# Performance work log

Measured on AMD Instinct MI355X. Metric: run time of the kernel, lower is better.

The kernel has to match this reference:

```python
import jax, jax.numpy as jnp
import numpy as np

B, S, D, H, DFF, L, V = 4, 1024, 512, 8, 2048, 6, 16000
DK = D // H


def _pos_encoding(seq, d):
    pos = jnp.arange(seq, dtype=jnp.float32)[:, None]
    div = 10000.0 ** (jnp.arange(0, d, 2, dtype=jnp.float32) / d)
    pe = jnp.zeros((seq, d), jnp.float32)
    pe = pe.at[:, ::2].set(jnp.sin(pos / div))
    pe = pe.at[:, 1::2].set(jnp.cos(pos / div))
    return pe


def _ln(x, g, b, eps=1e-5):
    mu = x.mean(-1, keepdims=True)
    var = ((x - mu) ** 2).mean(-1, keepdims=True)
    return g * (x - mu) / jnp.sqrt(var + eps) + b


def _mha(xq, xkv, w, b, mask):
    # w: [4, D, D] (q, k, v, out); b: [4, D]
    q = (xq @ w[0] + b[0]).reshape(B, -1, H, DK).transpose(0, 2, 1, 3)  # [B,H,Sq,DK]
    k = (xkv @ w[1] + b[1]).reshape(B, -1, H, DK).transpose(0, 2, 1, 3)
    v = (xkv @ w[2] + b[2]).reshape(B, -1, H, DK).transpose(0, 2, 1, 3)
    scores = jnp.einsum('bhqd,bhkd->bhqk', q, k) / jnp.sqrt(jnp.float32(DK))
    if mask is not None:
        scores = jnp.where(mask, -jnp.inf, scores)
    att = jax.nn.softmax(scores, axis=-1)
    out = jnp.einsum('bhqk,bhkd->bhqd', att, v).transpose(0, 2, 1, 3).reshape(B, -1, D)
    return out @ w[3] + b[3]


def setup_inputs() -> dict:
    key = jax.random.key(0)
    ks = jax.random.split(key, 16)
    f = lambda k, shape: jax.random.normal(k, shape, dtype=jnp.float32) * 0.02
    return {
        'src': jax.random.randint(ks[0], (B, S), 0, V, dtype=jnp.int32),
        'tgt': jax.random.randint(ks[1], (B, S), 0, V, dtype=jnp.int32),
        'tgt_mask': jnp.triu(jnp.ones((S, S), dtype=bool), k=1),  # True == masked
        'src_emb': f(ks[2], (V, D)),
        'tgt_emb': f(ks[3], (V, D)),
        'enc_attn_w': f(ks[4], (L, 4, D, D)), 'enc_attn_b': jnp.zeros((L, 4, D)),
        'enc_ffn_w1': f(ks[5], (L, D, DFF)), 'enc_ffn_b1': jnp.zeros((L, DFF)),
        'enc_ffn_w2': f(ks[6], (L, DFF, D)), 'enc_ffn_b2': jnp.zeros((L, D)),
        'enc_ln_g': jnp.ones((L, 2, D)), 'enc_ln_b': jnp.zeros((L, 2, D)),
        'dec_attn_w': f(ks[7], (L, 8, D, D)), 'dec_attn_b': jnp.zeros((L, 8, D)),
        'dec_ffn_w1': f(ks[8], (L, D, DFF)), 'dec_ffn_b1': jnp.zeros((L, DFF)),
        'dec_ffn_w2': f(ks[9], (L, DFF, D)), 'dec_ffn_b2': jnp.zeros((L, D)),
        'dec_ln_g': jnp.ones((L, 3, D)), 'dec_ln_b': jnp.zeros((L, 3, D)),
        'gen_w': f(ks[10], (D, V)), 'gen_b': jnp.zeros((V,)),
    }


def reference(src, tgt, tgt_mask, src_emb, tgt_emb,
              enc_attn_w, enc_attn_b, enc_ffn_w1, enc_ffn_b1, enc_ffn_w2, enc_ffn_b2,
              enc_ln_g, enc_ln_b,
              dec_attn_w, dec_attn_b, dec_ffn_w1, dec_ffn_b1, dec_ffn_w2, dec_ffn_b2,
              dec_ln_g, dec_ln_b, gen_w, gen_b):
    pe = _pos_encoding(S, D)
    # Encoder (dropout is identity in eval)
    x = src_emb[src] + pe
    for i in range(L):
        a = _mha(x, x, enc_attn_w[i], enc_attn_b[i], None)
        x = _ln(x + a, enc_ln_g[i, 0], enc_ln_b[i, 0])
        ff = jax.nn.relu(x @ enc_ffn_w1[i] + enc_ffn_b1[i]) @ enc_ffn_w2[i] + enc_ffn_b2[i]
        x = _ln(x + ff, enc_ln_g[i, 1], enc_ln_b[i, 1])
    # Decoder
    y = tgt_emb[tgt] + pe
    for i in range(L):
        a = _mha(y, y, dec_attn_w[i, :4], dec_attn_b[i, :4], tgt_mask)
        y = _ln(y + a, dec_ln_g[i, 0], dec_ln_b[i, 0])
        a = _mha(y, x, dec_attn_w[i, 4:], dec_attn_b[i, 4:], None)
        y = _ln(y + a, dec_ln_g[i, 1], dec_ln_b[i, 1])
        ff = jax.nn.relu(y @ dec_ffn_w1[i] + dec_ffn_b1[i]) @ dec_ffn_w2[i] + dec_ffn_b2[i]
        y = _ln(y + ff, dec_ln_g[i, 2], dec_ln_b[i, 2])
    # Generator (CrossEntropyLoss variant -> raw logits)
    return y @ gen_w + gen_b
```

## Files before the change

### kernel.cpp

```cpp
#include <hip/hip_runtime.h>
#include <hip/hip_bf16.h>
#include <math.h>

typedef __hip_bfloat16 bf16;
typedef __attribute__((ext_vector_type(8))) short          s16x8;
typedef __attribute__((ext_vector_type(8))) unsigned short u16x8;
typedef __attribute__((ext_vector_type(4))) float          f32x4;

#define B_   4
#define S_   1024
#define D_   512
#define H_   8
#define DK_  64
#define DFF_ 2048
#define L_   6
#define V_   16000
#define NT_  (B_ * S_)

__global__ void detect_kernel(const void* __restrict__ g, int* __restrict__ flag)
{
    const unsigned short* u = (const unsigned short*)g;
    *flag = (u[0] == 0x3F80 && u[1] == 0x3F80) ? 1 : 0;
}

__device__ __forceinline__ float ldw(const void* p, size_t i, int isbf)
{
    if (isbf) return __bfloat162float(((const bf16*)p)[i]);
    return ((const float*)p)[i];
}

__device__ __forceinline__ unsigned short f2b(float f)
{
    unsigned int u = __float_as_uint(f);
    return (unsigned short)((u + 0x7FFFu + ((u >> 16) & 1u)) >> 16);
}
__device__ __forceinline__ float b2f(unsigned short u)
{
    return __uint_as_float((unsigned int)u << 16);
}

__global__ __launch_bounds__(256)
void embed_kernel(const int* __restrict__ tok, const void* __restrict__ emb,
                  float* __restrict__ X, const int* __restrict__ flagp)
{
    const int isbf = *flagp;
    int idx = blockIdx.x * 256 + threadIdx.x;
    int d  = idx & (D_ - 1);
    int bs = idx >> 9;
    int s  = bs & (S_ - 1);
    int t  = tok[bs];
    float e = ldw(emb, (size_t)t * D_ + d, isbf);
    float expo = (float)(d & ~1) * (1.0f / (float)D_);
    float div  = powf(10000.0f, expo);
    float arg  = (float)s / div;
    float pe   = (d & 1) ? cosf(arg) : sinf(arg);
    X[idx] = e + pe;
}

__global__ __launch_bounds__(256)
void wconv_kernel(const void* __restrict__ W, unsigned short* __restrict__ Wt,
                  int K, int N, const int* __restrict__ flagp)
{
    __shared__ unsigned short T[64 * 72];
    const int isbf = *flagp;
    const int tid = threadIdx.x;
    const int n0 = blockIdx.x * 64, k0 = blockIdx.y * 64;
    const size_t mb = (size_t)blockIdx.z * K * N;
#pragma unroll
    for (int i = 0; i < 16; ++i) {
        int idx = i * 256 + tid;
        int kk = idx >> 6, n = idx & 63;
        unsigned short v;
        if (isbf) v = ((const unsigned short*)W)[mb + (size_t)(k0 + kk) * N + n0 + n];
        else      v = f2b(((const float*)W)[mb + (size_t)(k0 + kk) * N + n0 + n]);
        T[n * 72 + kk] = v;
    }
    __syncthreads();
#pragma unroll
    for (int j = 0; j < 2; ++j) {
        int unit = j * 256 + tid;
        int n = unit >> 3, q = unit & 7;
        *(u16x8*)&Wt[mb + (size_t)(n0 + n) * K + k0 + q * 8] =
            *(const u16x8*)&T[n * 72 + q * 8];
    }
}

template<int BM, int BN, int ABF, int WT, int OB>
__global__ __launch_bounds__(256)
void gemm2_kernel(const void* __restrict__ A,
                  const void* __restrict__ W, size_t w_off,
                  const void* __restrict__ bias, size_t b_off,
                  const float* __restrict__ res,
                  void* __restrict__ C, void* __restrict__ Cout,
                  int M, int N, int K, int relu,
                  size_t sW, size_t sO, size_t sB,
                  const int* __restrict__ flagp)
{
    constexpr int ROWU = 40;
    constexpr int FM = BM / 32;
    constexpr int FN = BN / 32;
    __shared__ __align__(16) unsigned short As[BM * ROWU];
    __shared__ __align__(16) unsigned short Bs[BN * ROWU];

    const int isbf = *flagp;
    const int tid  = threadIdx.x;
    const int lane = tid & 63;
    const int wid  = tid >> 6;
    const int wr   = wid >> 1, wc = wid & 1;
    const int l15  = lane & 15, g = lane >> 4;
    const int row0 = blockIdx.y * BM;
    const int col0 = blockIdx.x * BN;
    const int z    = blockIdx.z;
    const size_t wbase = w_off + (size_t)z * sW;

    f32x4 acc[FM][FN];
#pragma unroll
    for (int i = 0; i < FM; ++i)
#pragma unroll
        for (int j = 0; j < FN; ++j)
            acc[i][j] = (f32x4){0.f, 0.f, 0.f, 0.f};

    for (int k0 = 0; k0 < K; k0 += 32) {
        if (ABF) {
#pragma unroll
            for (int u = 0; u < BM / 64; ++u) {
                int unit = tid + u * 256;
                int r = unit >> 2, q = unit & 3;
                *(u16x8*)&As[r * ROWU + q * 8] = *(const u16x8*)
                    ((const unsigned short*)A + (size_t)(row0 + r) * K + k0 + q * 8);
            }
        } else {
#pragma unroll
            for (int u = 0; u < (BM * 4) / 256; ++u) {
                int unit = tid + u * 256;
                int r = unit >> 2, q = unit & 3;
                const float* ap = (const float*)A + (size_t)(row0 + r) * K + k0 + q * 8;
                float4 f0 = *(const float4*)ap;
                float4 f1 = *(const float4*)(ap + 4);
                u16x8 v;
                v[0] = f2b(f0.x); v[1] = f2b(f0.y); v[2] = f2b(f0.z); v[3] = f2b(f0.w);
                v[4] = f2b(f1.x); v[5] = f2b(f1.y); v[6] = f2b(f1.z); v[7] = f2b(f1.w);
                *(u16x8*)&As[r * ROWU + q * 8] = v;
            }
        }
        if (WT) {
#pragma unroll
            for (int u = 0; u < BN / 64; ++u) {
                int unit = tid + u * 256;
                int n = unit >> 2, q = unit & 3;
                *(u16x8*)&Bs[n * ROWU + q * 8] = *(const u16x8*)
                    ((const unsigned short*)W + wbase + (size_t)(col0 + n) * K + k0 + q * 8);
            }
        } else {
#pragma unroll
            for (int u = 0; u < (BN * 4) / 256; ++u) {
                int unit = tid + u * 256;
                int n = unit >> 2, q = unit & 3;
                u16x8 v;
                if (isbf) {
                    const unsigned short* wp = (const unsigned short*)W;
#pragma unroll
                    for (int j = 0; j < 8; ++j)
                        v[j] = wp[wbase + (size_t)(k0 + q * 8 + j) * N + col0 + n];
                } else {
                    const float* wp = (const float*)W;
#pragma unroll
                    for (int j = 0; j < 8; ++j)
                        v[j] = f2b(wp[wbase + (size_t)(k0 + q * 8 + j) * N + col0 + n]);
                }
                *(u16x8*)&Bs[n * ROWU + q * 8] = v;
            }
        }
        __syncthreads();

        s16x8 af[FM], bfr[FN];
#pragma unroll
        for (int mi = 0; mi < FM; ++mi) {
            int r = wr * (BM / 2) + mi * 16 + l15;
            af[mi] = *(const s16x8*)&As[r * ROWU + g * 8];
        }
#pragma unroll
        for (int ni = 0; ni < FN; ++ni) {
            int c = wc * (BN / 2) + ni * 16 + l15;
            bfr[ni] = *(const s16x8*)&Bs[c * ROWU + g * 8];
        }
#pragma unroll
        for (int mi = 0; mi < FM; ++mi)
#pragma unroll
            for (int ni = 0; ni < FN; ++ni)
                acc[mi][ni] = __builtin_amdgcn_mfma_f32_16x16x32_bf16(
                    af[mi], bfr[ni], acc[mi][ni], 0, 0, 0);
        __syncthreads();
    }

#pragma unroll
    for (int mi = 0; mi < FM; ++mi) {
#pragma unroll
        for (int ni = 0; ni < FN; ++ni) {
            int n = col0 + wc * (BN / 2) + ni * 16 + l15;
            float bv = ldw(bias, b_off + (size_t)z * sB + n, isbf);
#pragma unroll
            for (int q = 0; q < 4; ++q) {
                int m = row0 + wr * (BM / 2) + mi * 16 + g * 4 + q;
                float v = acc[mi][ni][q] + bv;
                size_t oidx = (size_t)m * N + n;
                if (res)  v += res[oidx];
                if (relu) v = fmaxf(v, 0.f);
                if (OB == 0)      ((float*)C + (size_t)z * sO)[oidx] = v;
                else if (OB == 1) ((unsigned short*)C + (size_t)z * sO)[oidx] = f2b(v);
                else {
                    if (isbf) ((bf16*)Cout)[oidx] = __float2bfloat16(v);
                    else      ((float*)Cout)[oidx] = v;
                }
            }
        }
    }
}

#define QBLK_ 64
#define KVB_  64
#define LROW_ 72

template<int CAUSAL>
__global__ __launch_bounds__(256)
void fattn_kernel(const unsigned short* __restrict__ Q,
                  const unsigned short* __restrict__ Kp,
                  const unsigned short* __restrict__ Vp,
                  unsigned short* __restrict__ O)
{
    __shared__ __align__(16) unsigned short Ks[64 * LROW_];
    __shared__ __align__(16) unsigned short Vt[64 * LROW_];
    __shared__ __align__(16) unsigned short QP[64 * LROW_];

    const int q0  = blockIdx.x * QBLK_;
    const int h   = blockIdx.y, b = blockIdx.z;
    const int tid = threadIdx.x;
    const int lane = tid & 63, w = tid >> 6;
    const int l15 = lane & 15, g = lane >> 4;

    {
        int r = tid >> 2, c = (tid & 3) * 16;
        const unsigned short* qp = Q + ((size_t)(b * S_ + q0 + r) * H_ + h) * DK_ + c;
        u16x8 v0 = *(const u16x8*)qp, v1 = *(const u16x8*)(qp + 8);
#pragma unroll
        for (int j = 0; j < 8; ++j) v0[j] = f2b(b2f(v0[j]) * 0.125f);
#pragma unroll
        for (int j = 0; j < 8; ++j) v1[j] = f2b(b2f(v1[j]) * 0.125f);
        *(u16x8*)&QP[r * LROW_ + c]     = v0;
        *(u16x8*)&QP[r * LROW_ + c + 8] = v1;
    }
    __syncthreads();
    s16x8 aq0 = *(const s16x8*)&QP[(w * 16 + l15) * LROW_ + g * 8];
    s16x8 aq1 = *(const s16x8*)&QP[(w * 16 + l15) * LROW_ + 32 + g * 8];

    float m[4] = {-INFINITY, -INFINITY, -INFINITY, -INFINITY};
    float l[4] = {0.f, 0.f, 0.f, 0.f};
    f32x4 o[4];
#pragma unroll
    for (int ni = 0; ni < 4; ++ni) o[ni] = (f32x4){0.f, 0.f, 0.f, 0.f};

    const int nt = CAUSAL ? (q0 / KVB_ + 1) : (S_ / KVB_);
    for (int t = 0; t < nt; ++t) {
        const int j0 = t * KVB_;
        {
            int r = tid >> 2, c = (tid & 3) * 16;
            const unsigned short* kp = Kp + ((size_t)(b * S_ + j0 + r) * H_ + h) * DK_ + c;
            *(u16x8*)&Ks[r * LROW_ + c]     = *(const u16x8*)kp;
            *(u16x8*)&Ks[r * LROW_ + c + 8] = *(const u16x8*)(kp + 8);
        }
        {
            int d = tid & 63, kq = tid >> 6;
            const unsigned short* vp = Vp + ((size_t)(b * S_ + j0 + kq * 16) * H_ + h) * DK_ + d;
            u16x8 v0, v1;
#pragma unroll
            for (int j = 0; j < 8; ++j) v0[j] = vp[(size_t)j * (H_ * DK_)];
#pragma unroll
            for (int j = 0; j < 8; ++j) v1[j] = vp[(size_t)(8 + j) * (H_ * DK_)];
            *(u16x8*)&Vt[d * LROW_ + kq * 16]     = v0;
            *(u16x8*)&Vt[d * LROW_ + kq * 16 + 8] = v1;
        }
        __syncthreads();

        f32x4 sc[4];
#pragma unroll
        for (int ni = 0; ni < 4; ++ni) {
            s16x8 bk0 = *(const s16x8*)&Ks[(ni * 16 + l15) * LROW_ + g * 8];
            s16x8 bk1 = *(const s16x8*)&Ks[(ni * 16 + l15) * LROW_ + 32 + g * 8];
            f32x4 a = (f32x4){0.f, 0.f, 0.f, 0.f};
            a = __builtin_amdgcn_mfma_f32_16x16x32_bf16(aq0, bk0, a, 0, 0, 0);
            a = __builtin_amdgcn_mfma_f32_16x16x32_bf16(aq1, bk1, a, 0, 0, 0);
            sc[ni] = a;
        }
        if (CAUSAL && (j0 + KVB_ > q0)) {
#pragma unroll
            for (int ni = 0; ni < 4; ++ni)
#pragma unroll
                for (int r = 0; r < 4; ++r) {
                    int qrow = q0 + w * 16 + g * 4 + r;
                    int col  = j0 + ni * 16 + l15;
                    if (col > qrow) sc[ni][r] = -INFINITY;
                }
        }
        float pr[4][4];
#pragma unroll
        for (int r = 0; r < 4; ++r) {
            float mt = fmaxf(fmaxf(sc[0][r], sc[1][r]), fmaxf(sc[2][r], sc[3][r]));
#pragma unroll
            for (int sft = 1; sft < 16; sft <<= 1)
                mt = fmaxf(mt, __shfl_xor(mt, sft, 64));
            float mn = fmaxf(m[r], mt);
            float rescale = __expf(m[r] - mn);
            float rs = 0.f;
#pragma unroll
            for (int ni = 0; ni < 4; ++ni) {
                float p = __expf(sc[ni][r] - mn);
                pr[ni][r] = p;
                rs += p;
            }
#pragma unroll
            for (int sft = 1; sft < 16; sft <<= 1)
                rs += __shfl_xor(rs, sft, 64);
            l[r] = l[r] * rescale + rs;
            m[r] = mn;
#pragma unroll
            for (int ni = 0; ni < 4; ++ni) o[ni][r] *= rescale;
        }
#pragma unroll
        for (int ni = 0; ni < 4; ++ni)
#pragma unroll
            for (int r = 0; r < 4; ++r)
                QP[(w * 16 + g * 4 + r) * LROW_ + ni * 16 + l15] = f2b(pr[ni][r]);
        s16x8 pa0 = *(const s16x8*)&QP[(w * 16 + l15) * LROW_ + g * 8];
        s16x8 pa1 = *(const s16x8*)&QP[(w * 16 + l15) * LROW_ + 32 + g * 8];
#pragma unroll
        for (int ni = 0; ni < 4; ++ni) {
            s16x8 vb0 = *(const s16x8*)&Vt[(ni * 16 + l15) * LROW_ + g * 8];
            s16x8 vb1 = *(const s16x8*)&Vt[(ni * 16 + l15) * LROW_ + 32 + g * 8];
            o[ni] = __builtin_amdgcn_mfma_f32_16x16x32_bf16(pa0, vb0, o[ni], 0, 0, 0);
            o[ni] = __builtin_amdgcn_mfma_f32_16x16x32_bf16(pa1, vb1, o[ni], 0, 0, 0);
        }
        __syncthreads();
    }

#pragma unroll
    for (int r = 0; r < 4; ++r) {
        float inv = 1.0f / l[r];
        int qrow = q0 + w * 16 + g * 4 + r;
        unsigned short* op = O + ((size_t)(b * S_ + qrow) * H_ + h) * DK_;
#pragma unroll
        for (int ni = 0; ni < 4; ++ni)
            op[ni * 16 + l15] = f2b(o[ni][r] * inv);
    }
}

__global__ __launch_bounds__(256)
void layernorm_kernel(const float* __restrict__ X,
                      const void* __restrict__ g, size_t g_off,
                      const void* __restrict__ bb, size_t b_off,
                      float* __restrict__ Y, const int* __restrict__ flagp)
{
    __shared__ float red[256];
    const int isbf = *flagp;
    const int row = blockIdx.x, tid = threadIdx.x;
    const float* x = X + (size_t)row * D_;
    float v0 = x[tid], v1 = x[tid + 256];
    red[tid] = v0 + v1;
    __syncthreads();
    for (int s = 128; s > 0; s >>= 1) {
        if (tid < s) red[tid] += red[tid + s];
        __syncthreads();
    }
    float mean = red[0] * (1.0f / (float)D_);
    __syncthreads();
    float d0 = v0 - mean, d1 = v1 - mean;
    red[tid] = d0 * d0 + d1 * d1;
    __syncthreads();
    for (int s = 128; s > 0; s >>= 1) {
        if (tid < s) red[tid] += red[tid + s];
        __syncthreads();
    }
    float r = rsqrtf(red[0] * (1.0f / (float)D_) + 1e-5f);
    float* y = Y + (size_t)row * D_;
    y[tid]       = ldw(g, g_off + tid, isbf)       * d0 * r + ldw(bb, b_off + tid, isbf);
    y[tid + 256] = ldw(g, g_off + tid + 256, isbf) * d1 * r + ldw(bb, b_off + tid + 256, isbf);
}

extern "C" void kernel_launch(void* const* d_in, const int* in_sizes, int n_in,
                              void* d_out, int out_size, void* d_ws, size_t ws_size,
                              hipStream_t stream)
{
    (void)in_sizes; (void)n_in; (void)out_size;

    const int*  src      = (const int*)d_in[0];
    const int*  tgt      = (const int*)d_in[1];
    const void* src_emb  = d_in[3];
    const void* tgt_emb  = d_in[4];
    const void* eaw      = d_in[5];
    const void* eab      = d_in[6];
    const void* ew1      = d_in[7];
    const void* eb1      = d_in[8];
    const void* ew2      = d_in[9];
    const void* eb2      = d_in[10];
    const void* elg      = d_in[11];
    const void* elb      = d_in[12];
    const void* daw      = d_in[13];
    const void* dab      = d_in[14];
    const void* dw1      = d_in[15];
    const void* db1      = d_in[16];
    const void* dw2      = d_in[17];
    const void* db2      = d_in[18];
    const void* dlg      = d_in[19];
    const void* dlb      = d_in[20];
    const void* gen_w    = d_in[21];
    const void* gen_b    = d_in[22];

    const size_t tokD = (size_t)NT_ * D_;
    const size_t tokF = (size_t)NT_ * DFF_;
    const size_t DD   = (size_t)D_ * D_;

    const size_t O_EAW = 0;
    const size_t O_EW1 = O_EAW + 24ULL * DD;
    const size_t O_EW2 = O_EW1 + 6ULL * D_ * DFF_;
    const size_t O_DAW = O_EW2 + 6ULL * DFF_ * D_;
    const size_t O_DW1 = O_DAW + 48ULL * DD;
    const size_t O_DW2 = O_DW1 + 6ULL * D_ * DFF_;
    const size_t O_GEN = O_DW2 + 6ULL * DFF_ * D_;
    const size_t WTELEMS = O_GEN + (size_t)D_ * V_;

    size_t off = 256;
    int*   flagp = (int*)d_ws;
    float* xbuf = (float*)((char*)d_ws + off); off += tokD * 4;
    float* ybuf = (float*)((char*)d_ws + off); off += tokD * 4;
    float* tbuf = (float*)((char*)d_ws + off); off += tokD * 4;
    unsigned short* qb = (unsigned short*)((char*)d_ws + off); off += tokD * 2;
    unsigned short* kb = (unsigned short*)((char*)d_ws + off); off += tokD * 2;
    unsigned short* vb = (unsigned short*)((char*)d_ws + off); off += tokD * 2;
    unsigned short* ab = (unsigned short*)((char*)d_ws + off); off += tokD * 2;
    unsigned short* fb = (unsigned short*)((char*)d_ws + off); off += tokF * 2;
    const size_t need_small = off;
    unsigned short* Wt = (unsigned short*)((char*)d_ws + off); off += WTELEMS * 2;
    const size_t need_big = off;

    if (ws_size < need_small) return;
    const bool big = (ws_size >= need_big);

    detect_kernel<<<1, 1, 0, stream>>>(elg, flagp);

    if (big) {
        auto wc = [&](const void* W, size_t dstoff, int K, int N, int z) {
            dim3 g(N / 64, K / 64, z);
            wconv_kernel<<<g, 256, 0, stream>>>(W, Wt + dstoff, K, N, flagp);
        };
        wc(eaw,   O_EAW, 512, 512,   24);
        wc(ew1,   O_EW1, 512, 2048,  6);
        wc(ew2,   O_EW2, 2048, 512,  6);
        wc(daw,   O_DAW, 512, 512,   48);
        wc(dw1,   O_DW1, 512, 2048,  6);
        wc(dw2,   O_DW2, 2048, 512,  6);
        wc(gen_w, O_GEN, 512, 16000, 1);
    }

    auto gP = [&](const float* A, const void* Wf, size_t roff, size_t woff,
                  const void* bias, size_t boff, unsigned short* C,
                  int N, int K, int nz, size_t sW, size_t sO, size_t sB) {
        dim3 grid(N / 64, NT_ / 64, nz);
        if (big) gemm2_kernel<64, 64, 0, 1, 1><<<grid, 256, 0, stream>>>(
            A, Wt, roff + woff, bias, boff, nullptr, C, nullptr,
            NT_, N, K, 0, sW, sO, sB, flagp);
        else     gemm2_kernel<64, 64, 0, 0, 1><<<grid, 256, 0, stream>>>(
            A, Wf, woff, bias, boff, nullptr, C, nullptr,
            NT_, N, K, 0, sW, sO, sB, flagp);
    };
    auto gO = [&](const unsigned short* A, const void* Wf, size_t roff, size_t woff,
                  const void* bias, size_t boff, const float* res, float* C,
                  int N, int K) {
        dim3 grid(N / 64, NT_ / 64, 1);
        if (big) gemm2_kernel<64, 64, 1, 1, 0><<<grid, 256, 0, stream>>>(
            A, Wt, roff + woff, bias, boff, res, C, nullptr,
            NT_, N, K, 0, 0, 0, 0, flagp);
        else     gemm2_kernel<64, 64, 1, 0, 0><<<grid, 256, 0, stream>>>(
            A, Wf, woff, bias, boff, res, C, nullptr,
            NT_, N, K, 0, 0, 0, 0, flagp);
    };
    auto gF1 = [&](const float* A, const void* Wf, size_t roff, size_t woff,
                   const void* bias, size_t boff, unsigned short* C) {
        dim3 grid(DFF_ / 128, NT_ / 128, 1);
        if (big) gemm2_kernel<128, 128, 0, 1, 1><<<grid, 256, 0, stream>>>(
            A, Wt, roff + woff, bias, boff, nullptr, C, nullptr,
            NT_, DFF_, D_, 1, 0, 0, 0, flagp);
        else     gemm2_kernel<128, 128, 0, 0, 1><<<grid, 256, 0, stream>>>(
            A, Wf, woff, bias, boff, nullptr, C, nullptr,
            NT_, DFF_, D_, 1, 0, 0, 0, flagp);
    };
    auto gG = [&](const float* A) {
        dim3 grid(V_ / 128, NT_ / 128, 1);
        if (big) gemm2_kernel<128, 128, 0, 1, 2><<<grid, 256, 0, stream>>>(
            A, Wt, O_GEN, gen_b, 0, nullptr, nullptr, d_out,
            NT_, V_, D_, 0, 0, 0, 0, flagp);
        else     gemm2_kernel<128, 128, 0, 0, 2><<<grid, 256, 0, stream>>>(
            A, gen_w, 0, gen_b, 0, nullptr, nullptr, d_out,
            NT_, V_, D_, 0, 0, 0, 0, flagp);
    };
    auto attn = [&](const unsigned short* Q, const unsigned short* Kq,
                    const unsigned short* Vq, unsigned short* Oq, int causal) {
        dim3 g(S_ / QBLK_, H_, B_);
        if (causal) fattn_kernel<1><<<g, 256, 0, stream>>>(Q, Kq, Vq, Oq);
        else        fattn_kernel<0><<<g, 256, 0, stream>>>(Q, Kq, Vq, Oq);
    };
    auto ln = [&](const float* X, const void* g_, size_t g_off,
                  const void* b_, size_t b_off, float* Y) {
        layernorm_kernel<<<NT_, 256, 0, stream>>>(X, g_, g_off, b_, b_off, Y, flagp);
    };

    embed_kernel<<<(NT_ * D_) / 256, 256, 0, stream>>>(src, src_emb, xbuf, flagp);
    embed_kernel<<<(NT_ * D_) / 256, 256, 0, stream>>>(tgt, tgt_emb, ybuf, flagp);

    for (int i = 0; i < L_; ++i) {
        size_t w0 = (size_t)i * 4 * DD;
        size_t b0 = (size_t)i * 4 * D_;
        gP(xbuf, eaw, O_EAW, w0, eab, b0, qb, D_, D_, 3, DD, tokD, D_);
        attn(qb, kb, vb, ab, 0);
        gO(ab, eaw, O_EAW, w0 + 3 * DD, eab, b0 + 3 * D_, xbuf, tbuf, D_, D_);
        ln(tbuf, elg, (size_t)(i * 2 + 0) * D_, elb, (size_t)(i * 2 + 0) * D_, xbuf);
        gF1(xbuf, ew1, O_EW1, (size_t)i * D_ * DFF_, eb1, (size_t)i * DFF_, fb);
        gO(fb, ew2, O_EW2, (size_t)i * DFF_ * D_, eb2, (size_t)i * D_, xbuf, tbuf, D_, DFF_);
        ln(tbuf, elg, (size_t)(i * 2 + 1) * D_, elb, (size_t)(i * 2 + 1) * D_, xbuf);
    }

    for (int i = 0; i < L_; ++i) {
        size_t w0 = (size_t)i * 8 * DD;
        size_t b0 = (size_t)i * 8 * D_;
        gP(ybuf, daw, O_DAW, w0, dab, b0, qb, D_, D_, 3, DD, tokD, D_);
        attn(qb, kb, vb, ab, 1);
        gO(ab, daw, O_DAW, w0 + 3 * DD, dab, b0 + 3 * D_, ybuf, tbuf, D_, D_);
        ln(tbuf, dlg, (size_t)(i * 3 + 0) * D_, dlb, (size_t)(i * 3 + 0) * D_, ybuf);
        gP(ybuf, daw, O_DAW, w0 + 4 * DD, dab, b0 + 4 * D_, qb, D_, D_, 1, 0, 0, 0);
        gP(xbuf, daw, O_DAW, w0 + 5 * DD, dab, b0 + 5 * D_, kb, D_, D_, 2, DD, tokD, D_);
        attn(qb, kb, vb, ab, 0);
        gO(ab, daw, O_DAW, w0 + 7 * DD, dab, b0 + 7 * D_, ybuf, tbuf, D_, D_);
        ln(tbuf, dlg, (size_t)(i * 3 + 1) * D_, dlb, (size_t)(i * 3 + 1) * D_, ybuf);
        gF1(ybuf, dw1, O_DW1, (size_t)i * D_ * DFF_, db1, (size_t)i * DFF_, fb);
        gO(fb, dw2, O_DW2, (size_t)i * DFF_ * D_, db2, (size_t)i * D_, ybuf, tbuf, D_, DFF_);
        ln(tbuf, dlg, (size_t)(i * 3 + 2) * D_, dlb, (size_t)(i * 3 + 2) * D_, ybuf);
    }

    gG(ybuf);
}
```

Measured before the change: 3.239 ms.

## Load GEMM tiles via global_load_lds with swizzled LDS and bf16 activation copies

Adds a new GEMM kernel that streams A and pre-transposed weight tiles straight into LDS with global_load_lds, using an XOR-style rotation swizzle in place of padded rows to avoid bank conflicts. Embedding and layernorm now also write a bf16 copy of their activations, so GEMMs read bf16 inputs and skip per-tile fp32-to-bf16 conversion. Grid ordering is swapped so consecutive blocks walk the M dimension, projection GEMMs use 128x64 tiles, and the FFN buffer is aliased over the q/k/v/attn buffers to shrink the workspace. The cost is extra bf16 stores in layernorm and embed, and reliance on the direct-to-LDS load path and its swizzle being correct.

```diff
diff --git a/kernel.cpp b/kernel.cpp
--- a/kernel.cpp
+++ b/kernel.cpp
@@ -39,9 +39,17 @@
     return __uint_as_float((unsigned int)u << 16);
 }
 
+__device__ __forceinline__ void gl_lds16(const unsigned short* g, unsigned short* l)
+{
+    __builtin_amdgcn_global_load_lds(
+        (const __attribute__((address_space(1))) unsigned int*)g,
+        (__attribute__((address_space(3))) unsigned int*)l, 16, 0, 0);
+}
+
 __global__ __launch_bounds__(256)
 void embed_kernel(const int* __restrict__ tok, const void* __restrict__ emb,
-                  float* __restrict__ X, const int* __restrict__ flagp)
+                  float* __restrict__ X, unsigned short* __restrict__ Xb,
+                  const int* __restrict__ flagp)
 {
     const int isbf = *flagp;
     int idx = blockIdx.x * 256 + threadIdx.x;
@@ -54,7 +62,9 @@
     float div  = powf(10000.0f, expo);
     float arg  = (float)s / div;
     float pe   = (d & 1) ? cosf(arg) : sinf(arg);
-    X[idx] = e + pe;
+    float v = e + pe;
+    X[idx]  = v;
+    Xb[idx] = f2b(v);
 }
 
 __global__ __launch_bounds__(256)
@@ -85,10 +95,10 @@
     }
 }
 
-template<int BM, int BN, int ABF, int WT, int OB>
+template<int BM, int BN, int OB>
 __global__ __launch_bounds__(256)
-void gemm2_kernel(const void* __restrict__ A,
-                  const void* __restrict__ W, size_t w_off,
+void gemm3_kernel(const unsigned short* __restrict__ A,
+                  const unsigned short* __restrict__ Wt, size_t w_off,
                   const void* __restrict__ bias, size_t b_off,
                   const float* __restrict__ res,
                   void* __restrict__ C, void* __restrict__ Cout,
@@ -96,20 +106,21 @@
                   size_t sW, size_t sO, size_t sB,
                   const int* __restrict__ flagp)
 {
-    constexpr int ROWU = 40;
     constexpr int FM = BM / 32;
     constexpr int FN = BN / 32;
-    __shared__ __align__(16) unsigned short As[BM * ROWU];
-    __shared__ __align__(16) unsigned short Bs[BN * ROWU];
+    __shared__ __align__(16) unsigned short As[BM * 32];
+    __shared__ __align__(16) unsigned short Bs[BN * 32];
 
     const int isbf = *flagp;
     const int tid  = threadIdx.x;
     const int lane = tid & 63;
-    const int wid  = tid >> 6;
-    const int wr   = wid >> 1, wc = wid & 1;
+    const int wv   = tid >> 6;
+    const int wr   = wv >> 1, wc = wv & 1;
     const int l15  = lane & 15, g = lane >> 4;
-    const int row0 = blockIdx.y * BM;
-    const int col0 = blockIdx.x * BN;
+    const int sr   = lane >> 2;
+    const int sp   = lane & 3;
+    const int row0 = blockIdx.x * BM;
+    const int col0 = blockIdx.y * BN;
     const int z    = blockIdx.z;
     const size_t wbase = w_off + (size_t)z * sW;
 
@@ -121,55 +132,19 @@
             acc[i][j] = (f32x4){0.f, 0.f, 0.f, 0.f};
 
     for (int k0 = 0; k0 < K; k0 += 32) {
-        if (ABF) {
-#pragma unroll
-            for (int u = 0; u < BM / 64; ++u) {
-                int unit = tid + u * 256;
-                int r = unit >> 2, q = unit & 3;
-                *(u16x8*)&As[r * ROWU + q * 8] = *(const u16x8*)
-                    ((const unsigned short*)A + (size_t)(row0 + r) * K + k0 + q * 8);
-            }
-        } else {
-#pragma unroll
-            for (int u = 0; u < (BM * 4) / 256; ++u) {
-                int unit = tid + u * 256;
-                int r = unit >> 2, q = unit & 3;
-                const float* ap = (const float*)A + (size_t)(row0 + r) * K + k0 + q * 8;
-                float4 f0 = *(const float4*)ap;
-                float4 f1 = *(const float4*)(ap + 4);
-                u16x8 v;
-                v[0] = f2b(f0.x); v[1] = f2b(f0.y); v[2] = f2b(f0.z); v[3] = f2b(f0.w);
-                v[4] = f2b(f1.x); v[5] = f2b(f1.y); v[6] = f2b(f1.z); v[7] = f2b(f1.w);
-                *(u16x8*)&As[r * ROWU + q * 8] = v;
-            }
-        }
-        if (WT) {
-#pragma unroll
-            for (int u = 0; u < BN / 64; ++u) {
-                int unit = tid + u * 256;
-                int n = unit >> 2, q = unit & 3;
-                *(u16x8*)&Bs[n * ROWU + q * 8] = *(const u16x8*)
-                    ((const unsigned short*)W + wbase + (size_t)(col0 + n) * K + k0 + q * 8);
-            }
-        } else {
-#pragma unroll
-            for (int u = 0; u < (BN * 4) / 256; ++u) {
-                int unit = tid + u * 256;
-                int n = unit >> 2, q = unit & 3;
-                u16x8 v;
-                if (isbf) {
-                    const unsigned short* wp = (const unsigned short*)W;
-#pragma unroll
-                    for (int j = 0; j < 8; ++j)
-                        v[j] = wp[wbase + (size_t)(k0 + q * 8 + j) * N + col0 + n];
-                } else {
-                    const float* wp = (const float*)W;
-#pragma unroll
-                    for (int j = 0; j < 8; ++j)
-                        v[j] = f2b(wp[wbase + (size_t)(k0 + q * 8 + j) * N + col0 + n]);
-                }
-                *(u16x8*)&Bs[n * ROWU + q * 8] = v;
-            }
+#pragma unroll
+        for (int u = 0; u < BM / 64; ++u) {
+            int r0 = u * 64 + wv * 16;
+            int r  = r0 + sr;
+            int q  = (sp - (r >> 1)) & 3;
+            gl_lds16(A + (size_t)(row0 + r) * K + k0 + q * 8, As + r0 * 32);
+        }
+#pragma unroll
+        for (int u = 0; u < BN / 64; ++u) {
+            int r0 = u * 64 + wv * 16;
+            int n  = r0 + sr;
+            int q  = (sp - (n >> 1)) & 3;
+            gl_lds16(Wt + wbase + (size_t)(col0 + n) * K + k0 + q * 8, Bs + r0 * 32);
         }
         __syncthreads();
 
@@ -177,12 +152,12 @@
 #pragma unroll
         for (int mi = 0; mi < FM; ++mi) {
             int r = wr * (BM / 2) + mi * 16 + l15;
-            af[mi] = *(const s16x8*)&As[r * ROWU + g * 8];
+            af[mi] = *(const s16x8*)&As[r * 32 + ((g + (r >> 1)) & 3) * 8];
         }
 #pragma unroll
         for (int ni = 0; ni < FN; ++ni) {
             int c = wc * (BN / 2) + ni * 16 + l15;
-            bfr[ni] = *(const s16x8*)&Bs[c * ROWU + g * 8];
+            bfr[ni] = *(const s16x8*)&Bs[c * 32 + ((g + (c >> 1)) & 3) * 8];
         }
 #pragma unroll
         for (int mi = 0; mi < FM; ++mi)
@@ -217,6 +192,113 @@
     }
 }
 
+template<int BM, int BN, int OB>
+__global__ __launch_bounds__(256)
+void gemm2_kernel(const unsigned short* __restrict__ A,
+                  const void* __restrict__ W, size_t w_off,
+                  const void* __restrict__ bias, size_t b_off,
+                  const float* __restrict__ res,
+                  void* __restrict__ C, void* __restrict__ Cout,
+                  int M, int N, int K, int relu,
+                  size_t sW, size_t sO, size_t sB,
+                  const int* __restrict__ flagp)
+{
+    constexpr int ROWU = 40;
+    constexpr int FM = BM / 32;
+    constexpr int FN = BN / 32;
+    __shared__ __align__(16) unsigned short As[BM * ROWU];
+    __shared__ __align__(16) unsigned short Bs[BN * ROWU];
+
+    const int isbf = *flagp;
+    const int tid  = threadIdx.x;
+    const int lane = tid & 63;
+    const int wid  = tid >> 6;
+    const int wr   = wid >> 1, wc = wid & 1;
+    const int l15  = lane & 15, g = lane >> 4;
+    const int row0 = blockIdx.y * BM;
+    const int col0 = blockIdx.x * BN;
+    const int z    = blockIdx.z;
+    const size_t wbase = w_off + (size_t)z * sW;
+
+    f32x4 acc[FM][FN];
+#pragma unroll
+    for (int i = 0; i < FM; ++i)
+#pragma unroll
+        for (int j = 0; j < FN; ++j)
+            acc[i][j] = (f32x4){0.f, 0.f, 0.f, 0.f};
+
+    for (int k0 = 0; k0 < K; k0 += 32) {
+#pragma unroll
+        for (int u = 0; u < BM / 64; ++u) {
+            int unit = tid + u * 256;
+            int r = unit >> 2, q = unit & 3;
+            *(u16x8*)&As[r * ROWU + q * 8] =
+                *(const u16x8*)(A + (size_t)(row0 + r) * K + k0 + q * 8);
+        }
+#pragma unroll
+        for (int u = 0; u < (BN * 4) / 256; ++u) {
+            int unit = tid + u * 256;
+            int n = unit >> 2, q = unit & 3;
+            u16x8 v;
+            if (isbf) {
+                const unsigned short* wp = (const unsigned short*)W;
+#pragma unroll
+                for (int j = 0; j < 8; ++j)
+                    v[j] = wp[wbase + (size_t)(k0 + q * 8 + j) * N + col0 + n];
+            } else {
+                const float* wp = (const float*)W;
+#pragma unroll
+                for (int j = 0; j < 8; ++j)
+                    v[j] = f2b(wp[wbase + (size_t)(k0 + q * 8 + j) * N + col0 + n]);
+            }
+            *(u16x8*)&Bs[n * ROWU + q * 8] = v;
+        }
+        __syncthreads();
+
+        s16x8 af[FM], bfr[FN];
+#pragma unroll
+        for (int mi = 0; mi < FM; ++mi) {
+            int r = wr * (BM / 2) + mi * 16 + l15;
+            af[mi] = *(const s16x8*)&As[r * ROWU + g * 8];
+        }
+#pragma unroll
+        for (int ni = 0; ni < FN; ++ni) {
+            int c = wc * (BN / 2) + ni * 16 + l15;
+            bfr[ni] = *(const s16x8*)&Bs[c * ROWU + g * 8];
+        }
+#pragma unroll
+        for (int mi = 0; mi < FM; ++mi)
+#pragma unroll
+            for (int ni = 0; ni < FN; ++ni)
+                acc[mi][ni] = __builtin_amdgcn_mfma_f32_16x16x32_bf16(
+                    af[mi], bfr[ni], acc[mi][ni], 0, 0, 0);
+        __syncthreads();
+    }
+
+#pragma unroll
+    for (int mi = 0; mi < FM; ++mi) {
+#pragma unroll
+        for (int ni = 0; ni < FN; ++ni) {
+            int n = col0 + wc * (BN / 2) + ni * 16 + l15;
+            float bv = ldw(bias, b_off + (size_t)z * sB + n, isbf);
+#pragma unroll
+            for (int q = 0; q < 4; ++q) {
+                int m = row0 + wr * (BM / 2) + mi * 16 + g * 4 + q;
+                float v = acc[mi][ni][q] + bv;
+                size_t oidx = (size_t)m * N + n;
+                if (res)  v += res[oidx];
+                if (relu) v = fmaxf(v, 0.f);
+                if (OB == 0)      ((float*)C + (size_t)z * sO)[oidx] = v;
+                else if (OB == 1) ((unsigned short*)C + (size_t)z * sO)[oidx] = f2b(v);
+                else {
+                    if (isbf) ((bf16*)Cout)[oidx] = __float2bfloat16(v);
+                    else      ((float*)Cout)[oidx] = v;
+                }
+            }
+        }
+    }
+}
+
 #define QBLK_ 64
 #define KVB_  64
 #define LROW_ 72
@@ -357,7 +439,8 @@
 void layernorm_kernel(const float* __restrict__ X,
                       const void* __restrict__ g, size_t g_off,
                       const void* __restrict__ bb, size_t b_off,
-                      float* __restrict__ Y, const int* __restrict__ flagp)
+                      float* __restrict__ Y, unsigned short* __restrict__ Yb,
+                      const int* __restrict__ flagp)
 {
     __shared__ float red[256];
     const int isbf = *flagp;
@@ -380,9 +463,14 @@
         __syncthreads();
     }
     float r = rsqrtf(red[0] * (1.0f / (float)D_) + 1e-5f);
+    float y0 = ldw(g, g_off + tid, isbf)       * d0 * r + ldw(bb, b_off + tid, isbf);
+    float y1 = ldw(g, g_off + tid + 256, isbf) * d1 * r + ldw(bb, b_off + tid + 256, isbf);
     float* y = Y + (size_t)row * D_;
-    y[tid]       = ldw(g, g_off + tid, isbf)       * d0 * r + ldw(bb, b_off + tid, isbf);
-    y[tid + 256] = ldw(g, g_off + tid + 256, isbf) * d1 * r + ldw(bb, b_off + tid + 256, isbf);
+    unsigned short* yb = Yb + (size_t)row * D_;
+    y[tid]        = y0;
+    y[tid + 256]  = y1;
+    yb[tid]       = f2b(y0);
+    yb[tid + 256] = f2b(y1);
 }
 
 extern "C" void kernel_launch(void* const* d_in, const int* in_sizes, int n_in,
@@ -432,11 +520,14 @@
     float* xbuf = (float*)((char*)d_ws + off); off += tokD * 4;
     float* ybuf = (float*)((char*)d_ws + off); off += tokD * 4;
     float* tbuf = (float*)((char*)d_ws + off); off += tokD * 4;
-    unsigned short* qb = (unsigned short*)((char*)d_ws + off); off += tokD * 2;
-    unsigned short* kb = (unsigned short*)((char*)d_ws + off); off += tokD * 2;
-    unsigned short* vb = (unsigned short*)((char*)d_ws + off); off += tokD * 2;
-    unsigned short* ab = (unsigned short*)((char*)d_ws + off); off += tokD * 2;
-    unsigned short* fb = (unsigned short*)((char*)d_ws + off); off += tokF * 2;
+    unsigned short* xb16 = (unsigned short*)((char*)d_ws + off); off += tokD * 2;
+    unsigned short* yb16 = (unsigned short*)((char*)d_ws + off); off += tokD * 2;
+    unsigned short* qb = (unsigned short*)((char*)d_ws + off);
+    unsigned short* fb = qb;
+    unsigned short* kb = qb + tokD;
+    unsigned short* vb = kb + tokD;
+    unsigned short* ab = vb + tokD;
+    off += tokF * 2;
     const size_t need_small = off;
     unsigned short* Wt = (unsigned short*)((char*)d_ws + off); off += WTELEMS * 2;
     const size_t need_big = off;
@@ -460,46 +551,61 @@
         wc(gen_w, O_GEN, 512, 16000, 1);
     }
 
-    auto gP = [&](const float* A, const void* Wf, size_t roff, size_t woff,
+    auto gP = [&](const unsigned short* A, const void* Wf, size_t roff, size_t woff,
                   const void* bias, size_t boff, unsigned short* C,
-                  int N, int K, int nz, size_t sW, size_t sO, size_t sB) {
-        dim3 grid(N / 64, NT_ / 64, nz);
-        if (big) gemm2_kernel<64, 64, 0, 1, 1><<<grid, 256, 0, stream>>>(
-            A, Wt, roff + woff, bias, boff, nullptr, C, nullptr,
-            NT_, N, K, 0, sW, sO, sB, flagp);
-        else     gemm2_kernel<64, 64, 0, 0, 1><<<grid, 256, 0, stream>>>(
-            A, Wf, woff, bias, boff, nullptr, C, nullptr,
-            NT_, N, K, 0, sW, sO, sB, flagp);
+                  int K, int nz, size_t sW, size_t sO, size_t sB) {
+        if (big) {
+            dim3 grid(NT_ / 128, 512 / 64, nz);
+            gemm3_kernel<128, 64, 1><<<grid, 256, 0, stream>>>(
+                A, Wt, roff + woff, bias, boff, nullptr, C, nullptr,
+                NT_, 512, K, 0, sW, sO, sB, flagp);
+        } else {
+            dim3 grid(512 / 64, NT_ / 64, nz);
+            gemm2_kernel<64, 64, 1><<<grid, 256, 0, stream>>>(
+                A, Wf, woff, bias, boff, nullptr, C, nullptr,
+                NT_, 512, K, 0, sW, sO, sB, flagp);
+        }
     };
     auto gO = [&](const unsigned short* A, const void* Wf, size_t roff, size_t woff,
-                  const void* bias, size_t boff, const float* res, float* C,
-                  int N, int K) {
-        dim3 grid(N / 64, NT_ / 64, 1);
-        if (big) gemm2_kernel<64, 64, 1, 1, 0><<<grid, 256, 0, stream>>>(
-            A, Wt, roff + woff, bias, boff, res, C, nullptr,
-            NT_, N, K, 0, 0, 0, 0, flagp);
-        else     gemm2_kernel<64, 64, 1, 0, 0><<<grid, 256, 0, stream>>>(
-            A, Wf, woff, bias, boff, res, C, nullptr,
-            NT_, N, K, 0, 0, 0, 0, flagp);
+                  const void* bias, size_t boff, const float* res, float* C, int K) {
+        if (big) {
+            dim3 grid(NT_ / 128, 512 / 64, 1);
+            gemm3_kernel<128, 64, 0><<<grid, 256, 0, stream>>>(
+                A, Wt, roff + woff, bias, boff, res, C, nullptr,
+                NT_, 512, K, 0, 0, 0, 0, flagp);
+        } else {
+            dim3 grid(512 / 64, NT_ / 64, 1);
+            gemm2_kernel<64, 64, 0><<<grid, 256, 0, stream>>>(
+                A, Wf, woff, bias, boff, res, C, nullptr,
+                NT_, 512, K, 0, 0, 0, 0, flagp);
+        }
     };
-    auto gF1 = [&](const float* A, const void* Wf, size_t roff, size_t woff,
+    auto gF1 = [&](const unsigned short* A, const void* Wf, size_t roff, size_t woff,
                    const void* bias, size_t boff, unsigned short* C) {
-        dim3 grid(DFF_ / 128, NT_ / 128, 1);
-        if (big) gemm2_kernel<128, 128, 0, 1, 1><<<grid, 256, 0, stream>>>(
-            A, Wt, roff + woff, bias, boff, nullptr, C, nullptr,
-            NT_, DFF_, D_, 1, 0, 0, 0, flagp);
-        else     gemm2_kernel<128, 128, 0, 0, 1><<<grid, 256, 0, stream>>>(
-            A, Wf, woff, bias, boff, nullptr, C, nullptr,
-            NT_, DFF_, D_, 1, 0, 0, 0, flagp);
+        if (big) {
+            dim3 grid(NT_ / 128, DFF_ / 128, 1);
+            gemm3_kernel<128, 128, 1><<<grid, 256, 0, stream>>>(
+                A, Wt, roff + woff, bias, boff, nullptr, C, nullptr,
+                NT_, DFF_, D_, 1, 0, 0, 0, flagp);
+        } else {
+            dim3 grid(DFF_ / 128, NT_ / 128, 1);
+            gemm2_kernel<128, 128, 1><<<grid, 256, 0, stream>>>(
+                A, Wf, woff, bias, boff, nullptr, C, nullptr,
+                NT_, DFF_, D_, 1, 0, 0, 0, flagp);
+        }
     };
-    auto gG = [&](const float* A) {
-        dim3 grid(V_ / 128, NT_ / 128, 1);
-        if (big) gemm2_kernel<128, 128, 0, 1, 2><<<grid, 256, 0, stream>>>(
-            A, Wt, O_GEN, gen_b, 0, nullptr, nullptr, d_out,
-            NT_, V_, D_, 0, 0, 0, 0, flagp);
-        else     gemm2_kernel<128, 128, 0, 0, 2><<<grid, 256, 0, stream>>>(
-            A, gen_w, 0, gen_b, 0, nullptr, nullptr, d_out,
-            NT_, V_, D_, 0, 0, 0, 0, flagp);
+    auto gG = [&](const unsigned short* A) {
+        if (big) {
+            dim3 grid(NT_ / 128, V_ / 128, 1);
+            gemm3_kernel<128, 128, 2><<<grid, 256, 0, stream>>>(
+                A, Wt, O_GEN, gen_b, 0, nullptr, nullptr, d_out,
+                NT_, V_, D_, 0, 0, 0, 0, flagp);
+        } else {
+            dim3 grid(V_ / 128, NT_ / 128, 1);
+            gemm2_kernel<128, 128, 2><<<grid, 256, 0, stream>>>(
+                A, gen_w, 0, gen_b, 0, nullptr, nullptr, d_out,
+                NT_, V_, D_, 0, 0, 0, 0, flagp);
+        }
     };
     auto attn = [&](const unsigned short* Q, const unsigned short* Kq,
                     const unsigned short* Vq, unsigned short* Oq, int causal) {
@@ -508,41 +614,41 @@
         else        fattn_kernel<0><<<g, 256, 0, stream>>>(Q, Kq, Vq, Oq);
     };
     auto ln = [&](const float* X, const void* g_, size_t g_off,
-                  const void* b_, size_t b_off, float* Y) {
-        layernorm_kernel<<<NT_, 256, 0, stream>>>(X, g_, g_off, b_, b_off, Y, flagp);
+                  const void* b_, size_t b_off, float* Y, unsigned short* Yb) {
+        layernorm_kernel<<<NT_, 256, 0, stream>>>(X, g_, g_off, b_, b_off, Y, Yb, flagp);
     };
 
-    embed_kernel<<<(NT_ * D_) / 256, 256, 0, stream>>>(src, src_emb, xbuf, flagp);
-    embed_kernel<<<(NT_ * D_) / 256, 256, 0, stream>>>(tgt, tgt_emb, ybuf, flagp);
+    embed_kernel<<<(NT_ * D_) / 256, 256, 0, stream>>>(src, src_emb, xbuf, xb16, flagp);
+    embed_kernel<<<(NT_ * D_) / 256, 256, 0, stream>>>(tgt, tgt_emb, ybuf, yb16, flagp);
 
     for (int i = 0; i < L_; ++i) {
         size_t w0 = (size_t)i * 4 * DD;
         size_t b0 = (size_t)i * 4 * D_;
-        gP(xbuf, eaw, O_EAW, w0, eab, b0, qb, D_, D_, 3, DD, tokD, D_);
+        gP(xb16, eaw, O_EAW, w0, eab, b0, qb, D_, 3, DD, tokD, D_);
         attn(qb, kb, vb, ab, 0);
-        gO(ab, eaw, O_EAW, w0 + 3 * DD, eab, b0 + 3 * D_, xbuf, tbuf, D_, D_);
-        ln(tbuf, elg, (size_t)(i * 2 + 0) * D_, elb, (size_t)(i * 2 + 0) * D_, xbuf);
-        gF1(xbuf, ew1, O_EW1, (size_t)i * D_ * DFF_, eb1, (size_t)i * DFF_, fb);
-        gO(fb, ew2, O_EW2, (size_t)i * DFF_ * D_, eb2, (size_t)i * D_, xbuf, tbuf, D_, DFF_);
-        ln(tbuf, elg, (size_t)(i * 2 + 1) * D_, elb, (size_t)(i * 2 + 1) * D_, xbuf);
+        gO(ab, eaw, O_EAW, w0 + 3 * DD, eab, b0 + 3 * D_, xbuf, tbuf, D_);
+        ln(tbuf, elg, (size_t)(i * 2 + 0) * D_, elb, (size_t)(i * 2 + 0) * D_, xbuf, xb16);
+        gF1(xb16, ew1, O_EW1, (size_t)i * D_ * DFF_, eb1, (size_t)i * DFF_, fb);
+        gO(fb, ew2, O_EW2, (size_t)i * DFF_ * D_, eb2, (size_t)i * D_, xbuf, tbuf, DFF_);
+        ln(tbuf, elg, (size_t)(i * 2 + 1) * D_, elb, (size_t)(i * 2 + 1) * D_, xbuf, xb16);
     }
 
     for (int i = 0; i < L_; ++i) {
         size_t w0 = (size_t)i * 8 * DD;
         size_t b0 = (size_t)i * 8 * D_;
-        gP(ybuf, daw, O_DAW, w0, dab, b0, qb, D_, D_, 3, DD, tokD, D_);
+        gP(yb16, daw, O_DAW, w0, dab, b0, qb, D_, 3, DD, tokD, D_);
         attn(qb, kb, vb, ab, 1);
-        gO(ab, daw, O_DAW, w0 + 3 * DD, dab, b0 + 3 * D_, ybuf, tbuf, D_, D_);
-        ln(tbuf, dlg, (size_t)(i * 3 + 0) * D_, dlb, (size_t)(i * 3 + 0) * D_, ybuf);
-        gP(ybuf, daw, O_DAW, w0 + 4 * DD, dab, b0 + 4 * D_, qb, D_, D_, 1, 0, 0, 0);
-        gP(xbuf, daw, O_DAW, w0 + 5 * DD, dab, b0 + 5 * D_, kb, D_, D_, 2, DD, tokD, D_);
+        gO(ab, daw, O_DAW, w0 + 3 * DD, dab, b0 + 3 * D_, ybuf, tbuf, D_);
+        ln(tbuf, dlg, (size_t)(i * 3 + 0) * D_, dlb, (size_t)(i * 3 + 0) * D_, ybuf, yb16);
+        gP(yb16, daw, O_DAW, w0 + 4 * DD, dab, b0 + 4 * D_, qb, D_, 1, 0, 0, 0);
+        gP(xb16, daw, O_DAW, w0 + 5 * DD, dab, b0 + 5 * D_, kb, D_, 2, DD, tokD, D_);
         attn(qb, kb, vb, ab, 0);
-        gO(ab, daw, O_DAW, w0 + 7 * DD, dab, b0 + 7 * D_, ybuf, tbuf, D_, D_);
-        ln(tbuf, dlg, (size_t)(i * 3 + 1) * D_, dlb, (size_t)(i * 3 + 1) * D_, ybuf);
-        gF1(ybuf, dw1, O_DW1, (size_t)i * D_ * DFF_, db1, (size_t)i * DFF_, fb);
-        gO(fb, dw2, O_DW2, (size_t)i * DFF_ * D_, db2, (size_t)i * D_, ybuf, tbuf, D_, DFF_);
-        ln(tbuf, dlg, (size_t)(i * 3 + 2) * D_, dlb, (size_t)(i * 3 + 2) * D_, ybuf);
-    }
-
-    gG(ybuf);
-}
+        gO(ab, daw, O_DAW, w0 + 7 * DD, dab, b0 + 7 * D_, ybuf, tbuf, D_);
+        ln(tbuf, dlg, (size_t)(i * 3 + 1) * D_, dlb, (size_t)(i * 3 + 1) * D_, ybuf, yb16);
+        gF1(yb16, dw1, O_DW1, (size_t)i * D_ * DFF_, db1, (size_t)i * DFF_, fb);
+        gO(fb, dw2, O_DW2, (size_t)i * DFF_ * D_, db2, (size_t)i * D_, ybuf, tbuf, DFF_);
+        ln(tbuf, dlg, (size_t)(i * 3 + 2) * D_, dlb, (size_t)(i * 3 + 2) * D_, ybuf, yb16);
+    }
+
+    gG(yb16);
+}
```

New measurement: 3.176 ms. 1.02x faster.
